# Optimization experiments

Hardware: AMD Instinct MI355X
Metric: run time of the kernel (lower is better)

Reference implementation:

```python
import jax, jax.numpy as jnp
import numpy as np

PAD = float(-2**32 + 1)
NUM_HEADS = 16
LN_EPS = 1e-5


def _split_heads(x, h):
    # torch.cat(torch.chunk(x, h, dim=2), dim=0): head-major stacking
    B, T, D = x.shape
    d = D // h
    return x.reshape(B, T, h, d).transpose(2, 0, 1, 3).reshape(h * B, T, d)


def _merge_heads(x, h):
    # torch.cat(torch.chunk(x, h, dim=0), dim=2)
    hB, T, d = x.shape
    B = hB // h
    return x.reshape(h, B, T, d).transpose(1, 2, 0, 3).reshape(B, T, h * d)


def setup_inputs() -> dict:
    key = jax.random.key(0)
    ks = jax.random.split(key, 12)
    B, T, D = 2, 2048, 1024
    s = 1.0 / np.sqrt(D)
    return {
        "q": jax.random.normal(ks[0], (B, T, D), jnp.float32),
        "k": jax.random.normal(ks[1], (B, T, D), jnp.float32),
        "v": jax.random.normal(ks[2], (B, T, D), jnp.float32),
        "mask": jax.random.randint(ks[3], (B, T), 0, 2, jnp.int32),
        "causality": 0,
        "edge_fea": jnp.zeros((1,), jnp.float32),
        "wq": jax.random.normal(ks[4], (D, D), jnp.float32) * s,
        "bq": jax.random.normal(ks[5], (D,), jnp.float32) * 0.01,
        "wk": jax.random.normal(ks[6], (D, D), jnp.float32) * s,
        "bk": jax.random.normal(ks[7], (D,), jnp.float32) * 0.01,
        "wv": jax.random.normal(ks[8], (D, D), jnp.float32) * s,
        "bv": jax.random.normal(ks[9], (D,), jnp.float32) * 0.01,
        "gamma": jnp.ones((D,), jnp.float32),
        "beta": jnp.zeros((D,), jnp.float32),
    }


def reference(q, k, v, mask, causality, edge_fea, wq, bq, wk, bk, wv, bv, gamma, beta):
    h = NUM_HEADS
    B, T, D = q.shape
    depth = D // h

    qh = _split_heads(q @ wq.T + bq, h)   # (h*B, T, depth)
    kh = _split_heads(k @ wk.T + bk, h)
    vh = _split_heads(v @ wv.T + bv, h)

    scores = jnp.einsum('ntd,nsd->nts', qh, kh) / jnp.sqrt(jnp.asarray(depth, qh.dtype))
    # key mask: repeat_interleave over dim 0 (batch-major), 1 => masked
    km = jnp.repeat(mask.astype(scores.dtype), h, axis=0)[:, None, :]  # (h*B,1,T)
    scores = scores + km * PAD
    if causality:
        tril = jnp.tril(jnp.ones((T, T), scores.dtype))
        scores = jnp.where(tril[None] == 0, jnp.full_like(scores, PAD), scores)
    attn = jax.nn.softmax(scores, axis=-1)
    ctx = jnp.einsum('nts,nsd->ntd', attn, vh)

    out = _merge_heads(ctx, h) + q  # dropout is identity in eval mode
    # LayerNorm over last dim
    mu = jnp.mean(out, axis=-1, keepdims=True)
    var = jnp.var(out, axis=-1, keepdims=True)
    out = (out - mu) / jnp.sqrt(var + LN_EPS) * gamma + beta
    return out
```

## Files before the change

kernel.cpp:

```cpp
#include <hip/hip_runtime.h>
#include <hip/hip_bf16.h>
#include <stdint.h>

#define B_ 2
#define T_ 2048
#define D_ 1024
#define H_ 16
#define DEPTH 64

typedef unsigned short u16;
typedef unsigned int u32;
typedef short bf16x8 __attribute__((ext_vector_type(8)));
typedef float f32x4 __attribute__((ext_vector_type(4)));

#define MFMA16(a, b, c) __builtin_amdgcn_mfma_f32_16x16x32_bf16(a, b, c, 0, 0, 0)

#define GLOAD_LDS(g, l)                                                      \
    __builtin_amdgcn_global_load_lds(                                        \
        (__attribute__((address_space(1))) void*)(g),                        \
        (__attribute__((address_space(3))) void*)(l), 16, 0, 0)

__device__ __forceinline__ u16 f2bf(float f) {
    union { float f; u32 i; } x; x.f = f;
    u32 r = x.i + 0x7fffu + ((x.i >> 16) & 1u);
    return (u16)(r >> 16);
}
__device__ __forceinline__ uint2 pk4(float4 f) {
    return make_uint2((u32)f2bf(f.x) | ((u32)f2bf(f.y) << 16),
                      (u32)f2bf(f.z) | ((u32)f2bf(f.w) << 16));
}
__device__ __forceinline__ u32 pkfast(float a, float b) {
    union { float f; u32 i; } x, y; x.f = a; y.f = b;
    return ((y.i + 0x8000u) & 0xffff0000u) | ((x.i + 0x8000u) >> 16);
}

__global__ __launch_bounds__(256) void conv_kernel(
    const float* __restrict__ s0, const float* __restrict__ s1, const float* __restrict__ s2,
    const float* __restrict__ s3, const float* __restrict__ s4, const float* __restrict__ s5,
    u16* __restrict__ xbf, u16* __restrict__ wbf)
{
    const int z = blockIdx.y;
    const float* src = (z == 0) ? s0 : (z == 1) ? s1 : (z == 2) ? s2
                     : (z == 3) ? s3 : (z == 4) ? s4 : s5;
    u16* dst = (z < 3) ? (xbf + (size_t)z * 4194304) : (wbf + (size_t)(z - 3) * 1048576);
    const size_t nel = (z < 3) ? 4194304u : 1048576u;
    for (size_t i = ((size_t)blockIdx.x * 256 + threadIdx.x) * 8; i < nel;
         i += (size_t)gridDim.x * 2048) {
        float4 a = *(const float4*)(src + i);
        float4 b = *(const float4*)(src + i + 4);
        uint2 lo = pk4(a), hi = pk4(b);
        *(uint4*)(dst + i) = make_uint4(lo.x, lo.y, hi.x, hi.y);
    }
}

__global__ __launch_bounds__(256, 3) void proj_mfma(
    const u16* __restrict__ xbf, const u16* __restrict__ wbf,
    const float* __restrict__ bq, const float* __restrict__ bk, const float* __restrict__ bv,
    u16* __restrict__ qh, u16* __restrict__ kh, u16* __restrict__ vt)
{
    __shared__ __attribute__((aligned(16))) u16 As[128 * 64];
    __shared__ __attribute__((aligned(16))) u16 Bs[128 * 64];

    const int z = blockIdx.z;
    const u16* A = xbf + (size_t)z * 4194304;
    const u16* W = wbf + (size_t)z * 1048576;
    const float* bias = (z == 0) ? bq : (z == 1) ? bk : bv;

    const int tid = threadIdx.x, w = tid >> 6, lane = tid & 63;
    const int quad = lane >> 4, l16 = lane & 15;
    const int m0 = blockIdx.y * 128, n0 = blockIdx.x * 128;
    const int wm = (w & 1) * 64, wn = (w >> 1) * 64;
    const int srow = lane >> 3;
    const int schunk = (lane & 7) ^ srow;

    f32x4 acc[4][4];
    #pragma unroll
    for (int mi = 0; mi < 4; ++mi)
        #pragma unroll
        for (int ni = 0; ni < 4; ++ni) acc[mi][ni] = (f32x4){0.f, 0.f, 0.f, 0.f};

    const size_t ar = (size_t)(m0 + 32 * w + srow);
    const size_t br = (size_t)(n0 + 32 * w + srow);

    for (int k0 = 0; k0 < D_; k0 += 64) {
        __syncthreads();
        #pragma unroll
        for (int i = 0; i < 4; ++i) {
            GLOAD_LDS(A + (ar + 8 * i) * D_ + k0 + schunk * 8, &As[(32 * w + 8 * i) * 64]);
            GLOAD_LDS(W + (br + 8 * i) * D_ + k0 + schunk * 8, &Bs[(32 * w + 8 * i) * 64]);
        }
        __syncthreads();

        #pragma unroll
        for (int kg = 0; kg < 2; ++kg) {
            const int ch = ((4 * kg + quad) ^ (l16 & 7)) * 8;
            bf16x8 af[4], bf[4];
            #pragma unroll
            for (int mi = 0; mi < 4; ++mi)
                af[mi] = *(const bf16x8*)&As[(wm + 16 * mi + l16) * 64 + ch];
            #pragma unroll
            for (int ni = 0; ni < 4; ++ni)
                bf[ni] = *(const bf16x8*)&Bs[(wn + 16 * ni + l16) * 64 + ch];
            #pragma unroll
            for (int mi = 0; mi < 4; ++mi)
                #pragma unroll
                for (int ni = 0; ni < 4; ++ni)
                    acc[mi][ni] = MFMA16(af[mi], bf[ni], acc[mi][ni]);
        }
    }

    float bl[4];
    #pragma unroll
    for (int ni = 0; ni < 4; ++ni) bl[ni] = bias[n0 + wn + ni * 16 + l16];

    #pragma unroll
    for (int mi = 0; mi < 4; ++mi) {
        const int mb = m0 + wm + mi * 16 + quad * 4;
        #pragma unroll
        for (int ni = 0; ni < 4; ++ni) {
            const int nn = n0 + wn + ni * 16 + l16;
            const int head = nn >> 6, d = nn & 63;
            if (z < 2) {
                u16* outp = (z == 0) ? qh : kh;
                #pragma unroll
                for (int r = 0; r < 4; ++r) {
                    const int m = mb + r;
                    const int b = m >> 11, t = m & (T_ - 1);
                    outp[((size_t)(head * B_ + b) * T_ + t) * DEPTH + d] =
                        f2bf(acc[mi][ni][r] + bl[ni]);
                }
            } else {
                const int b = mb >> 11, t = mb & (T_ - 1);
                float4 f = make_float4(acc[mi][ni][0] + bl[ni], acc[mi][ni][1] + bl[ni],
                                       acc[mi][ni][2] + bl[ni], acc[mi][ni][3] + bl[ni]);
                *(uint2*)(vt + ((size_t)(head * B_ + b) * DEPTH + d) * T_ + t) = pk4(f);
            }
        }
    }
}

__global__ __launch_bounds__(256, 4) void attn_kernel(
    const u16* __restrict__ qh, const u16* __restrict__ kh, const u16* __restrict__ vt,
    const int* __restrict__ maskp, const int* __restrict__ causp,
    float* __restrict__ outp)
{
    __shared__ __attribute__((aligned(16))) u16 Ks[64 * 64];
    __shared__ __attribute__((aligned(16))) u16 Vs[64 * 64];
    __shared__ __attribute__((aligned(16))) u16 Ps[4][2][16][72];
    __shared__ __attribute__((aligned(16))) float padf[T_];

    const int n  = blockIdx.y;
    const int qt = blockIdx.x;
    const int head = n >> 1, bi = n & 1;
    const int mrow = n >> 4;
    const int caus = causp[0];

    const int tid  = threadIdx.x;
    const int w    = tid >> 6, lane = tid & 63;
    const int quad = lane >> 4, l16 = lane & 15;
    const size_t base = (size_t)n * T_ * DEPTH;
    const size_t vbase = (size_t)n * DEPTH * T_;

    const float C1  = 0.18033688011112042f;
    const float PL2 = -6.2e9f;

    {
        const int i0 = tid * 8;
        int4 ma = *(const int4*)(maskp + (size_t)mrow * T_ + i0);
        int4 mb = *(const int4*)(maskp + (size_t)mrow * T_ + i0 + 4);
        padf[i0 + 0] = (float)ma.x * PL2; padf[i0 + 1] = (float)ma.y * PL2;
        padf[i0 + 2] = (float)ma.z * PL2; padf[i0 + 3] = (float)ma.w * PL2;
        padf[i0 + 4] = (float)mb.x * PL2; padf[i0 + 5] = (float)mb.y * PL2;
        padf[i0 + 6] = (float)mb.z * PL2; padf[i0 + 7] = (float)mb.w * PL2;
    }

    bf16x8 aq[2][2];
    #pragma unroll
    for (int s = 0; s < 2; ++s) {
        const int qg = qt * 128 + w * 32 + s * 16 + l16;
        aq[s][0] = *(const bf16x8*)(qh + base + (size_t)qg * DEPTH + quad * 8);
        aq[s][1] = *(const bf16x8*)(qh + base + (size_t)qg * DEPTH + 32 + quad * 8);
    }

    f32x4 O[2][4];
    #pragma unroll
    for (int s = 0; s < 2; ++s)
        #pragma unroll
        for (int t = 0; t < 4; ++t) O[s][t] = (f32x4){0.f, 0.f, 0.f, 0.f};
    float lp[2] = {0.f, 0.f};

    const int g_row = w * 16 + (lane >> 3);
    const int g_ch  = (lane & 7) ^ ((lane >> 3) & 7);
    const u16* ksrc = kh + base + (size_t)g_row * DEPTH + g_ch * 8;
    const u16* vsrc = vt + vbase + (size_t)g_row * T_ + g_ch * 8;

    for (int t0 = 0; t0 < T_; t0 += 64) {
        __syncthreads();
        GLOAD_LDS(ksrc + (size_t)t0 * DEPTH,           &Ks[(w * 16) * 64]);
        GLOAD_LDS(ksrc + (size_t)(t0 + 8) * DEPTH,     &Ks[(w * 16 + 8) * 64]);
        GLOAD_LDS(vsrc + t0,                           &Vs[(w * 16) * 64]);
        GLOAD_LDS(vsrc + (size_t)8 * T_ + t0,          &Vs[(w * 16 + 8) * 64]);
        __syncthreads();

        #pragma unroll
        for (int t = 0; t < 4; ++t) {
            const int krow = t * 16 + l16;
            const int swz = (l16 & 7);
            bf16x8 kb0 = *(const bf16x8*)&Ks[krow * 64 + ((quad ^ swz) * 8)];
            bf16x8 kb1 = *(const bf16x8*)&Ks[krow * 64 + (((4 + quad) ^ swz) * 8)];
            f32x4 pv4 = *(const f32x4*)&padf[t0 + t * 16 + quad * 4];
            #pragma unroll
            for (int s = 0; s < 2; ++s) {
                f32x4 st = (f32x4){0.f, 0.f, 0.f, 0.f};
                st = MFMA16(kb0, aq[s][0], st);
                st = MFMA16(kb1, aq[s][1], st);
                float v0 = fmaf(st[0], C1, pv4[0]);
                float v1 = fmaf(st[1], C1, pv4[1]);
                float v2 = fmaf(st[2], C1, pv4[2]);
                float v3 = fmaf(st[3], C1, pv4[3]);
                if (caus) {
                    const int kg = t0 + t * 16 + quad * 4;
                    const int qg = qt * 128 + w * 32 + s * 16 + l16;
                    if (kg + 0 > qg) v0 = PL2;
                    if (kg + 1 > qg) v1 = PL2;
                    if (kg + 2 > qg) v2 = PL2;
                    if (kg + 3 > qg) v3 = PL2;
                }
                const float e0 = exp2f(v0), e1 = exp2f(v1);
                const float e2 = exp2f(v2), e3 = exp2f(v3);
                lp[s] += (e0 + e1) + (e2 + e3);
                *(uint2*)&Ps[w][s][l16][t * 16 + quad * 4] =
                    make_uint2(pkfast(e0, e1), pkfast(e2, e3));
            }
        }

        bf16x8 ap[2][2];
        #pragma unroll
        for (int s = 0; s < 2; ++s) {
            ap[s][0] = *(const bf16x8*)&Ps[w][s][l16][quad * 8];
            ap[s][1] = *(const bf16x8*)&Ps[w][s][l16][32 + quad * 8];
        }
        #pragma unroll
        for (int t = 0; t < 4; ++t) {
            const int drow = t * 16 + l16;
            const int swz = (l16 & 7);
            bf16x8 vb0 = *(const bf16x8*)&Vs[drow * 64 + ((quad ^ swz) * 8)];
            bf16x8 vb1 = *(const bf16x8*)&Vs[drow * 64 + (((4 + quad) ^ swz) * 8)];
            #pragma unroll
            for (int s = 0; s < 2; ++s) {
                O[s][t] = MFMA16(ap[s][0], vb0, O[s][t]);
                O[s][t] = MFMA16(ap[s][1], vb1, O[s][t]);
            }
        }
    }

    #pragma unroll
    for (int s = 0; s < 2; ++s) {
        lp[s] += __shfl_xor(lp[s], 16, 64);
        lp[s] += __shfl_xor(lp[s], 32, 64);
    }

    #pragma unroll
    for (int s = 0; s < 2; ++s) {
        #pragma unroll
        for (int r = 0; r < 4; ++r) {
            const float lr  = __shfl(lp[s], quad * 4 + r, 64);
            const float inv = 1.0f / fmaxf(lr, 1e-30f);
            const size_t rb = ((size_t)bi * T_ + qt * 128 + w * 32 + s * 16 + quad * 4 + r) * D_
                            + head * DEPTH + l16;
            outp[rb + 0]  = O[s][0][r] * inv;
            outp[rb + 16] = O[s][1][r] * inv;
            outp[rb + 32] = O[s][2][r] * inv;
            outp[rb + 48] = O[s][3][r] * inv;
        }
    }
}

__global__ __launch_bounds__(256) void ln_kernel(
    const float* __restrict__ qin,
    const float* __restrict__ gamma, const float* __restrict__ beta,
    float* __restrict__ out)
{
    const int row = blockIdx.x;
    const int tid = threadIdx.x;
    const size_t basei = (size_t)row * D_ + (tid << 2);
    float4 c  = *(const float4*)(out + basei);
    float4 qv = *(const float4*)(qin + basei);
    float x[4] = {c.x + qv.x, c.y + qv.y, c.z + qv.z, c.w + qv.w};
    float s  = x[0] + x[1] + x[2] + x[3];
    float s2 = x[0]*x[0] + x[1]*x[1] + x[2]*x[2] + x[3]*x[3];
    #pragma unroll
    for (int off = 1; off < 64; off <<= 1) {
        s  += __shfl_xor(s, off, 64);
        s2 += __shfl_xor(s2, off, 64);
    }
    __shared__ float rs[4], rs2[4];
    const int wid = tid >> 6;
    if ((tid & 63) == 0) { rs[wid] = s; rs2[wid] = s2; }
    __syncthreads();
    s  = rs[0] + rs[1] + rs[2] + rs[3];
    s2 = rs2[0] + rs2[1] + rs2[2] + rs2[3];
    const float mean = s * (1.0f / (float)D_);
    const float var  = s2 * (1.0f / (float)D_) - mean * mean;
    const float rstd = rsqrtf(var + 1e-5f);
    float4 g = *(const float4*)(gamma + (tid << 2));
    float4 b = *(const float4*)(beta + (tid << 2));
    float4 r;
    r.x = (x[0] - mean) * rstd * g.x + b.x;
    r.y = (x[1] - mean) * rstd * g.y + b.y;
    r.z = (x[2] - mean) * rstd * g.z + b.z;
    r.w = (x[3] - mean) * rstd * g.w + b.w;
    *(float4*)(out + basei) = r;
}

extern "C" void kernel_launch(void* const* d_in, const int* in_sizes, int n_in,
                              void* d_out, int out_size, void* d_ws, size_t ws_size,
                              hipStream_t stream)
{
    (void)in_sizes; (void)n_in; (void)out_size; (void)ws_size;
    const float* q    = (const float*)d_in[0];
    const float* k    = (const float*)d_in[1];
    const float* v    = (const float*)d_in[2];
    const int* mask = (const int*)d_in[3];
    const int* caus = (const int*)d_in[4];
    const float* wq = (const float*)d_in[6];
    const float* bq = (const float*)d_in[7];
    const float* wk = (const float*)d_in[8];
    const float* bk = (const float*)d_in[9];
    const float* wv = (const float*)d_in[10];
    const float* bv = (const float*)d_in[11];
    const float* gamma = (const float*)d_in[12];
    const float* beta  = (const float*)d_in[13];
    float* out = (float*)d_out;

    const size_t elems = (size_t)B_ * T_ * D_;
    u16* qh  = (u16*)d_ws;
    u16* kh  = qh + elems;
    u16* vt  = kh + elems;
    u16* xbf = vt + elems;
    u16* wbf = xbf + 3 * elems;

    conv_kernel<<<dim3(512, 6), 256, 0, stream>>>(q, k, v, wq, wk, wv, xbf, wbf);
    proj_mfma<<<dim3(8, 32, 3), 256, 0, stream>>>(xbf, wbf, bq, bk, bv, qh, kh, vt);

    dim3 agrid(T_ / 128, H_ * B_);
    attn_kernel<<<agrid, 256, 0, stream>>>(qh, kh, vt, mask, caus, out);

    ln_kernel<<<B_ * T_, 256, 0, stream>>>(q, gamma, beta, out);
}
```

Before: 249.6 us.

## Double-buffer LDS tiles in projection and attention kernels to overlap loads

Both the QKV projection GEMM and the attention kernel now keep two LDS buffers for their K/V or A/W tiles. The next tile's global-to-LDS load is issued before computing on the current tile, and one barrier per iteration is removed, so memory latency can hide behind MFMA work. LDS use per block doubles for these tiles, and the launch bounds are lowered to 2 blocks per CU. That may reduce occupancy but leaves more registers per thread. Correctness relies on the top-of-loop barrier waiting for outstanding async loads.

After: 257.8 us. 3.3% more time.

```diff
diff --git a/kernel.cpp b/kernel.cpp
--- a/kernel.cpp
+++ b/kernel.cpp
@@ -53,13 +53,13 @@
     }
 }
 
-__global__ __launch_bounds__(256, 3) void proj_mfma(
+__global__ __launch_bounds__(256, 2) void proj_mfma(
     const u16* __restrict__ xbf, const u16* __restrict__ wbf,
     const float* __restrict__ bq, const float* __restrict__ bk, const float* __restrict__ bv,
     u16* __restrict__ qh, u16* __restrict__ kh, u16* __restrict__ vt)
 {
-    __shared__ __attribute__((aligned(16))) u16 As[128 * 64];
-    __shared__ __attribute__((aligned(16))) u16 Bs[128 * 64];
+    __shared__ __attribute__((aligned(16))) u16 As[2][128 * 64];
+    __shared__ __attribute__((aligned(16))) u16 Bs[2][128 * 64];
 
     const int z = blockIdx.z;
     const u16* A = xbf + (size_t)z * 4194304;
@@ -82,14 +82,23 @@
     const size_t ar = (size_t)(m0 + 32 * w + srow);
     const size_t br = (size_t)(n0 + 32 * w + srow);
 
+#define PROJ_STAGE(K0, BUF)                                                   \
+    {                                                                         \
+        _Pragma("unroll")                                                     \
+        for (int i_ = 0; i_ < 4; ++i_) {                                      \
+            GLOAD_LDS(A + (ar + 8 * i_) * D_ + (K0) + schunk * 8,             \
+                      &As[(BUF)][(32 * w + 8 * i_) * 64]);                    \
+            GLOAD_LDS(W + (br + 8 * i_) * D_ + (K0) + schunk * 8,             \
+                      &Bs[(BUF)][(32 * w + 8 * i_) * 64]);                    \
+        }                                                                     \
+    }
+
+    PROJ_STAGE(0, 0);
+
     for (int k0 = 0; k0 < D_; k0 += 64) {
+        const int cur = (k0 >> 6) & 1;
         __syncthreads();
-        #pragma unroll
-        for (int i = 0; i < 4; ++i) {
-            GLOAD_LDS(A + (ar + 8 * i) * D_ + k0 + schunk * 8, &As[(32 * w + 8 * i) * 64]);
-            GLOAD_LDS(W + (br + 8 * i) * D_ + k0 + schunk * 8, &Bs[(32 * w + 8 * i) * 64]);
-        }
-        __syncthreads();
+        if (k0 + 64 < D_) PROJ_STAGE(k0 + 64, cur ^ 1);
 
         #pragma unroll
         for (int kg = 0; kg < 2; ++kg) {
@@ -97,10 +106,10 @@
             bf16x8 af[4], bf[4];
             #pragma unroll
             for (int mi = 0; mi < 4; ++mi)
-                af[mi] = *(const bf16x8*)&As[(wm + 16 * mi + l16) * 64 + ch];
+                af[mi] = *(const bf16x8*)&As[cur][(wm + 16 * mi + l16) * 64 + ch];
             #pragma unroll
             for (int ni = 0; ni < 4; ++ni)
-                bf[ni] = *(const bf16x8*)&Bs[(wn + 16 * ni + l16) * 64 + ch];
+                bf[ni] = *(const bf16x8*)&Bs[cur][(wn + 16 * ni + l16) * 64 + ch];
             #pragma unroll
             for (int mi = 0; mi < 4; ++mi)
                 #pragma unroll
@@ -108,6 +117,7 @@
                     acc[mi][ni] = MFMA16(af[mi], bf[ni], acc[mi][ni]);
         }
     }
+#undef PROJ_STAGE
 
     float bl[4];
     #pragma unroll
@@ -139,13 +149,13 @@
     }
 }
 
-__global__ __launch_bounds__(256, 4) void attn_kernel(
+__global__ __launch_bounds__(256, 2) void attn_kernel(
     const u16* __restrict__ qh, const u16* __restrict__ kh, const u16* __restrict__ vt,
     const int* __restrict__ maskp, const int* __restrict__ causp,
     float* __restrict__ outp)
 {
-    __shared__ __attribute__((aligned(16))) u16 Ks[64 * 64];
-    __shared__ __attribute__((aligned(16))) u16 Vs[64 * 64];
+    __shared__ __attribute__((aligned(16))) u16 Ks[2][64 * 64];
+    __shared__ __attribute__((aligned(16))) u16 Vs[2][64 * 64];
     __shared__ __attribute__((aligned(16))) u16 Ps[4][2][16][72];
     __shared__ __attribute__((aligned(16))) float padf[T_];
 
@@ -194,20 +204,27 @@
     const u16* ksrc = kh + base + (size_t)g_row * DEPTH + g_ch * 8;
     const u16* vsrc = vt + vbase + (size_t)g_row * T_ + g_ch * 8;
 
+#define ATTN_STAGE(T0, BUF)                                                   \
+    {                                                                         \
+        GLOAD_LDS(ksrc + (size_t)(T0) * DEPTH,       &Ks[(BUF)][(w * 16) * 64]);     \
+        GLOAD_LDS(ksrc + (size_t)((T0) + 8) * DEPTH, &Ks[(BUF)][(w * 16 + 8) * 64]); \
+        GLOAD_LDS(vsrc + (T0),                       &Vs[(BUF)][(w * 16) * 64]);     \
+        GLOAD_LDS(vsrc + (size_t)8 * T_ + (T0),      &Vs[(BUF)][(w * 16 + 8) * 64]); \
+    }
+
+    ATTN_STAGE(0, 0);
+
     for (int t0 = 0; t0 < T_; t0 += 64) {
+        const int cur = (t0 >> 6) & 1;
         __syncthreads();
-        GLOAD_LDS(ksrc + (size_t)t0 * DEPTH,           &Ks[(w * 16) * 64]);
-        GLOAD_LDS(ksrc + (size_t)(t0 + 8) * DEPTH,     &Ks[(w * 16 + 8) * 64]);
-        GLOAD_LDS(vsrc + t0,                           &Vs[(w * 16) * 64]);
-        GLOAD_LDS(vsrc + (size_t)8 * T_ + t0,          &Vs[(w * 16 + 8) * 64]);
-        __syncthreads();
-
+        if (t0 + 64 < T_) ATTN_STAGE(t0 + 64, cur ^ 1);
+
+        const int swz = (l16 & 7);
         #pragma unroll
         for (int t = 0; t < 4; ++t) {
             const int krow = t * 16 + l16;
-            const int swz = (l16 & 7);
-            bf16x8 kb0 = *(const bf16x8*)&Ks[krow * 64 + ((quad ^ swz) * 8)];
-            bf16x8 kb1 = *(const bf16x8*)&Ks[krow * 64 + (((4 + quad) ^ swz) * 8)];
+            bf16x8 kb0 = *(const bf16x8*)&Ks[cur][krow * 64 + ((quad ^ swz) * 8)];
+            bf16x8 kb1 = *(const bf16x8*)&Ks[cur][krow * 64 + (((4 + quad) ^ swz) * 8)];
             f32x4 pv4 = *(const f32x4*)&padf[t0 + t * 16 + quad * 4];
             #pragma unroll
             for (int s = 0; s < 2; ++s) {
@@ -243,9 +260,8 @@
         #pragma unroll
         for (int t = 0; t < 4; ++t) {
             const int drow = t * 16 + l16;
-            const int swz = (l16 & 7);
-            bf16x8 vb0 = *(const bf16x8*)&Vs[drow * 64 + ((quad ^ swz) * 8)];
-            bf16x8 vb1 = *(const bf16x8*)&Vs[drow * 64 + (((4 + quad) ^ swz) * 8)];
+            bf16x8 vb0 = *(const bf16x8*)&Vs[cur][drow * 64 + ((quad ^ swz) * 8)];
+            bf16x8 vb1 = *(const bf16x8*)&Vs[cur][drow * 64 + (((4 + quad) ^ swz) * 8)];
             #pragma unroll
             for (int s = 0; s < 2; ++s) {
                 O[s][t] = MFMA16(ap[s][0], vb0, O[s][t]);
@@ -253,6 +269,7 @@
             }
         }
     }
+#undef ATTN_STAGE
 
     #pragma unroll
     for (int s = 0; s < 2; ++s) {
```

## Split attention over key halves and merge partials inside the layernorm kernel

Applied to the files above, without the earlier changes.

Each query tile's key range is split into two halves along a new grid dimension, which doubles the number of attention blocks (512 to 1024). Each half writes unnormalized bf16 partial outputs and row sums to workspace. The layernorm kernel now adds the two partials, divides by the combined sum and adds the residual. This gives better occupancy across compute units, at the cost of extra partial-output traffic and bf16 rounding of the unnormalized context. The merge is only valid because the softmax uses no running max, so the partial sums add directly.

Measured after the change: 234.1 us. -6.2%, faster.

```diff
diff --git a/kernel.cpp b/kernel.cpp
--- a/kernel.cpp
+++ b/kernel.cpp
@@ -20,6 +20,9 @@
         (__attribute__((address_space(1))) void*)(g),                        \
         (__attribute__((address_space(3))) void*)(l), 16, 0, 0)
 
+__device__ __forceinline__ float bf2f(u32 u) {
+    union { u32 i; float f; } x; x.i = u << 16; return x.f;
+}
 __device__ __forceinline__ u16 f2bf(float f) {
     union { float f; u32 i; } x; x.f = f;
     u32 r = x.i + 0x7fffu + ((x.i >> 16) & 1u);
@@ -142,15 +145,17 @@
 __global__ __launch_bounds__(256, 4) void attn_kernel(
     const u16* __restrict__ qh, const u16* __restrict__ kh, const u16* __restrict__ vt,
     const int* __restrict__ maskp, const int* __restrict__ causp,
-    float* __restrict__ outp)
+    u16* __restrict__ po, float* __restrict__ pl)
 {
     __shared__ __attribute__((aligned(16))) u16 Ks[64 * 64];
     __shared__ __attribute__((aligned(16))) u16 Vs[64 * 64];
     __shared__ __attribute__((aligned(16))) u16 Ps[4][2][16][72];
-    __shared__ __attribute__((aligned(16))) float padf[T_];
+    __shared__ __attribute__((aligned(16))) float padf[1024];
 
     const int n  = blockIdx.y;
     const int qt = blockIdx.x;
+    const int kk = blockIdx.z;
+    const int kbase = kk * 1024;
     const int head = n >> 1, bi = n & 1;
     const int mrow = n >> 4;
     const int caus = causp[0];
@@ -160,18 +165,16 @@
     const int quad = lane >> 4, l16 = lane & 15;
     const size_t base = (size_t)n * T_ * DEPTH;
     const size_t vbase = (size_t)n * DEPTH * T_;
+    const size_t elems = (size_t)B_ * T_ * D_;
 
     const float C1  = 0.18033688011112042f;
     const float PL2 = -6.2e9f;
 
     {
-        const int i0 = tid * 8;
-        int4 ma = *(const int4*)(maskp + (size_t)mrow * T_ + i0);
-        int4 mb = *(const int4*)(maskp + (size_t)mrow * T_ + i0 + 4);
-        padf[i0 + 0] = (float)ma.x * PL2; padf[i0 + 1] = (float)ma.y * PL2;
-        padf[i0 + 2] = (float)ma.z * PL2; padf[i0 + 3] = (float)ma.w * PL2;
-        padf[i0 + 4] = (float)mb.x * PL2; padf[i0 + 5] = (float)mb.y * PL2;
-        padf[i0 + 6] = (float)mb.z * PL2; padf[i0 + 7] = (float)mb.w * PL2;
+        const int i0 = tid * 4;
+        int4 m = *(const int4*)(maskp + (size_t)mrow * T_ + kbase + i0);
+        padf[i0 + 0] = (float)m.x * PL2; padf[i0 + 1] = (float)m.y * PL2;
+        padf[i0 + 2] = (float)m.z * PL2; padf[i0 + 3] = (float)m.w * PL2;
     }
 
     bf16x8 aq[2][2];
@@ -194,21 +197,22 @@
     const u16* ksrc = kh + base + (size_t)g_row * DEPTH + g_ch * 8;
     const u16* vsrc = vt + vbase + (size_t)g_row * T_ + g_ch * 8;
 
-    for (int t0 = 0; t0 < T_; t0 += 64) {
+    for (int t0 = kbase; t0 < kbase + 1024; t0 += 64) {
         __syncthreads();
-        GLOAD_LDS(ksrc + (size_t)t0 * DEPTH,           &Ks[(w * 16) * 64]);
-        GLOAD_LDS(ksrc + (size_t)(t0 + 8) * DEPTH,     &Ks[(w * 16 + 8) * 64]);
-        GLOAD_LDS(vsrc + t0,                           &Vs[(w * 16) * 64]);
-        GLOAD_LDS(vsrc + (size_t)8 * T_ + t0,          &Vs[(w * 16 + 8) * 64]);
+        GLOAD_LDS(ksrc + (size_t)t0 * DEPTH,       &Ks[(w * 16) * 64]);
+        GLOAD_LDS(ksrc + (size_t)(t0 + 8) * DEPTH, &Ks[(w * 16 + 8) * 64]);
+        GLOAD_LDS(vsrc + t0,                       &Vs[(w * 16) * 64]);
+        GLOAD_LDS(vsrc + (size_t)8 * T_ + t0,      &Vs[(w * 16 + 8) * 64]);
         __syncthreads();
 
+        const int swz = (l16 & 7);
+        const int lt0 = t0 - kbase;
         #pragma unroll
         for (int t = 0; t < 4; ++t) {
             const int krow = t * 16 + l16;
-            const int swz = (l16 & 7);
             bf16x8 kb0 = *(const bf16x8*)&Ks[krow * 64 + ((quad ^ swz) * 8)];
             bf16x8 kb1 = *(const bf16x8*)&Ks[krow * 64 + (((4 + quad) ^ swz) * 8)];
-            f32x4 pv4 = *(const f32x4*)&padf[t0 + t * 16 + quad * 4];
+            f32x4 pv4 = *(const f32x4*)&padf[lt0 + t * 16 + quad * 4];
             #pragma unroll
             for (int s = 0; s < 2; ++s) {
                 f32x4 st = (f32x4){0.f, 0.f, 0.f, 0.f};
@@ -243,7 +247,6 @@
         #pragma unroll
         for (int t = 0; t < 4; ++t) {
             const int drow = t * 16 + l16;
-            const int swz = (l16 & 7);
             bf16x8 vb0 = *(const bf16x8*)&Vs[drow * 64 + ((quad ^ swz) * 8)];
             bf16x8 vb1 = *(const bf16x8*)&Vs[drow * 64 + (((4 + quad) ^ swz) * 8)];
             #pragma unroll
@@ -254,39 +257,56 @@
         }
     }
 
+    u16* pop = po + (size_t)kk * elems;
+    float* plp = pl + (size_t)kk * 32 * T_;
     #pragma unroll
     for (int s = 0; s < 2; ++s) {
         lp[s] += __shfl_xor(lp[s], 16, 64);
         lp[s] += __shfl_xor(lp[s], 32, 64);
+        if (quad == 0)
+            plp[(size_t)n * T_ + qt * 128 + w * 32 + s * 16 + l16] = lp[s];
     }
 
     #pragma unroll
     for (int s = 0; s < 2; ++s) {
         #pragma unroll
         for (int r = 0; r < 4; ++r) {
-            const float lr  = __shfl(lp[s], quad * 4 + r, 64);
-            const float inv = 1.0f / fmaxf(lr, 1e-30f);
-            const size_t rb = ((size_t)bi * T_ + qt * 128 + w * 32 + s * 16 + quad * 4 + r) * D_
-                            + head * DEPTH + l16;
-            outp[rb + 0]  = O[s][0][r] * inv;
-            outp[rb + 16] = O[s][1][r] * inv;
-            outp[rb + 32] = O[s][2][r] * inv;
-            outp[rb + 48] = O[s][3][r] * inv;
-        }
-    }
-}
-
-__global__ __launch_bounds__(256) void ln_kernel(
+            const int qg = qt * 128 + w * 32 + s * 16 + quad * 4 + r;
+            const size_t rb = ((size_t)bi * T_ + qg) * D_ + head * DEPTH + l16;
+            pop[rb + 0]  = f2bf(O[s][0][r]);
+            pop[rb + 16] = f2bf(O[s][1][r]);
+            pop[rb + 32] = f2bf(O[s][2][r]);
+            pop[rb + 48] = f2bf(O[s][3][r]);
+        }
+    }
+}
+
+__global__ __launch_bounds__(256) void fuse_ln(
+    const u16* __restrict__ po, const float* __restrict__ pl,
     const float* __restrict__ qin,
     const float* __restrict__ gamma, const float* __restrict__ beta,
     float* __restrict__ out)
 {
     const int row = blockIdx.x;
+    const int bi = row >> 11, t = row & (T_ - 1);
     const int tid = threadIdx.x;
+    const size_t elems = (size_t)B_ * T_ * D_;
+
+    const int head = tid >> 4;
+    const size_t li = (size_t)(head * B_ + bi) * T_ + t;
+    const float l = pl[li] + pl[32 * T_ + li];
+    const float inv = 1.0f / fmaxf(l, 1e-30f);
+
     const size_t basei = (size_t)row * D_ + (tid << 2);
-    float4 c  = *(const float4*)(out + basei);
+    uint2 a = *(const uint2*)(po + basei);
+    uint2 b = *(const uint2*)(po + elems + basei);
     float4 qv = *(const float4*)(qin + basei);
-    float x[4] = {c.x + qv.x, c.y + qv.y, c.z + qv.z, c.w + qv.w};
+    float x[4];
+    x[0] = (bf2f(a.x & 0xffffu) + bf2f(b.x & 0xffffu)) * inv + qv.x;
+    x[1] = (bf2f(a.x >> 16)     + bf2f(b.x >> 16))     * inv + qv.y;
+    x[2] = (bf2f(a.y & 0xffffu) + bf2f(b.y & 0xffffu)) * inv + qv.z;
+    x[3] = (bf2f(a.y >> 16)     + bf2f(b.y >> 16))     * inv + qv.w;
+
     float s  = x[0] + x[1] + x[2] + x[3];
     float s2 = x[0]*x[0] + x[1]*x[1] + x[2]*x[2] + x[3]*x[3];
     #pragma unroll
@@ -304,12 +324,12 @@
     const float var  = s2 * (1.0f / (float)D_) - mean * mean;
     const float rstd = rsqrtf(var + 1e-5f);
     float4 g = *(const float4*)(gamma + (tid << 2));
-    float4 b = *(const float4*)(beta + (tid << 2));
+    float4 bb = *(const float4*)(beta + (tid << 2));
     float4 r;
-    r.x = (x[0] - mean) * rstd * g.x + b.x;
-    r.y = (x[1] - mean) * rstd * g.y + b.y;
-    r.z = (x[2] - mean) * rstd * g.z + b.z;
-    r.w = (x[3] - mean) * rstd * g.w + b.w;
+    r.x = (x[0] - mean) * rstd * g.x + bb.x;
+    r.y = (x[1] - mean) * rstd * g.y + bb.y;
+    r.z = (x[2] - mean) * rstd * g.z + bb.z;
+    r.w = (x[3] - mean) * rstd * g.w + bb.w;
     *(float4*)(out + basei) = r;
 }
 
@@ -339,12 +359,14 @@
     u16* vt  = kh + elems;
     u16* xbf = vt + elems;
     u16* wbf = xbf + 3 * elems;
+    u16* po   = xbf;
+    float* pl = (float*)(po + 2 * elems);
 
     conv_kernel<<<dim3(512, 6), 256, 0, stream>>>(q, k, v, wq, wk, wv, xbf, wbf);
     proj_mfma<<<dim3(8, 32, 3), 256, 0, stream>>>(xbf, wbf, bq, bk, bv, qh, kh, vt);
 
-    dim3 agrid(T_ / 128, H_ * B_);
-    attn_kernel<<<agrid, 256, 0, stream>>>(qh, kh, vt, mask, caus, out);
-
-    ln_kernel<<<B_ * T_, 256, 0, stream>>>(q, gamma, beta, out);
-}
+    dim3 agrid(T_ / 128, H_ * B_, 2);
+    attn_kernel<<<agrid, 256, 0, stream>>>(qh, kh, vt, mask, caus, po, pl);
+
+    fuse_ln<<<B_ * T_, 256, 0, stream>>>(po, pl, q, gamma, beta, out);
+}
```
